# Kernel optimization log

Measured on AMD Instinct MI355X. Metric: run time of the kernel, lower is better.

## Reference

```python
import jax, jax.numpy as jnp
import numpy as np
import math

# IPA hyperparameters (AlphaFold2 / ProtSeed defaults)
H, C, PQ, PV = 12, 16, 4, 8
CS, CZ = 384, 128
INF, EPS = 1e5, 1e-8
CAT = H * (CZ + C + 4 * PV)  # 2112


def setup_inputs() -> dict:
    key = jax.random.key(0)
    ks = jax.random.split(key, 20)
    B, N = 1, 512
    s = jax.random.normal(ks[0], (B, N, CS), jnp.float32)
    z = jax.random.normal(ks[1], (B, N, N, CZ), jnp.float32)
    # valid rotation matrices via QR of random gaussians
    rot = jnp.linalg.qr(jax.random.normal(ks[2], (B, N, 3, 3), jnp.float32))[0]
    trans = jax.random.normal(ks[3], (B, N, 3), jnp.float32)
    mask = jnp.ones((B, N), jnp.float32)
    sc = 0.02
    params = {
        'w_q': jax.random.normal(ks[4], (CS, H * C), jnp.float32) * sc,
        'b_q': jnp.zeros((H * C,), jnp.float32),
        'w_kv': jax.random.normal(ks[5], (CS, 2 * H * C), jnp.float32) * sc,
        'b_kv': jnp.zeros((2 * H * C,), jnp.float32),
        'w_qp': jax.random.normal(ks[6], (CS, H * PQ * 3), jnp.float32) * sc,
        'b_qp': jnp.zeros((H * PQ * 3,), jnp.float32),
        'w_kvp': jax.random.normal(ks[7], (CS, H * (PQ + PV) * 3), jnp.float32) * sc,
        'b_kvp': jnp.zeros((H * (PQ + PV) * 3,), jnp.float32),
        'w_b': jax.random.normal(ks[8], (CZ, H), jnp.float32) * sc,
        'b_b': jnp.zeros((H,), jnp.float32),
        'head_weights': jnp.full((H,), 0.5414, jnp.float32),  # softplus^-1(1)
        'w_out': jax.random.normal(ks[9], (CAT, CS), jnp.float32) * sc,
        'b_out': jnp.zeros((CS,), jnp.float32),
    }
    return {'s': s, 'z': z, 'rot': rot, 'trans': trans, 'mask': mask, **params}


def reference(s, z, rot, trans, mask, w_q, b_q, w_kv, b_kv, w_qp, b_qp,
              w_kvp, b_kvp, w_b, b_b, head_weights, w_out, b_out):
    B, N, _ = s.shape
    w_c = math.sqrt(1.0 / (3 * C))
    w_l = math.sqrt(1.0 / 3)
    w_p = math.sqrt(1.0 / (3 * (PQ * 9.0 / 2)))

    # scalar q/k/v: [B,N,H,C]
    q = (s @ w_q + b_q).reshape(B, N, H, C)
    kv = (s @ w_kv + b_kv).reshape(B, N, H, 2 * C)
    k, v = kv[..., :C], kv[..., C:]

    # point q/k/v in global frame. torch splits the projection into 3 chunks
    # (x,y,z) along the channel dim then stacks -> [B,N,H*P,3]
    def to_pts(w, b, p):
        pts = jnp.stack(jnp.split(s @ w + b, 3, axis=-1), axis=-1)  # [B,N,H*p,3]
        pts = jnp.einsum('bnij,bnpj->bnpi', rot, pts) + trans[:, :, None, :]
        return pts.reshape(B, N, H, p, 3)

    q_pts = to_pts(w_qp, b_qp, PQ)
    kv_pts = to_pts(w_kvp, b_kvp, PQ + PV)
    k_pts, v_pts = kv_pts[..., :PQ, :], kv_pts[..., PQ:, :]

    # pair bias [B,N,N,H]
    bias = z @ w_b + b_b

    # scalar attention logits [B,H,i,j]
    a = jnp.einsum('bihc,bjhc->bhij', q, k) * w_c
    a = a + w_l * jnp.transpose(bias, (0, 3, 1, 2))

    # point-distance term: [B,i,j,H,PQ]
    d2 = jnp.sum((q_pts[:, :, None] - k_pts[:, None]) ** 2, axis=-1)
    hw = jax.nn.softplus(head_weights) * w_p
    pt_att = -0.5 * jnp.sum(d2 * hw[None, None, None, :, None], axis=-1)  # [B,i,j,H]
    a = a + jnp.transpose(pt_att, (0, 3, 1, 2))

    sq_mask = INF * (mask[:, :, None] * mask[:, None, :] - 1.0)  # [B,i,j]
    a = jax.nn.softmax(a + sq_mask[:, None], axis=-1)  # [B,H,i,j]

    # scalar output [B,N,H*C]
    o = jnp.einsum('bhij,bjhc->bihc', a, v).reshape(B, N, H * C)

    # point output, mapped back to local frames: [B,i,H,PV,3]
    o_pt = jnp.einsum('bhij,bjhpx->bihpx', a, v_pts)
    o_pt = jnp.einsum('bnji,bnhpj->bnhpi', rot, o_pt - trans[:, :, None, None, :])
    o_pt_norm = jnp.sqrt(jnp.sum(o_pt ** 2, axis=-1) + EPS).reshape(B, N, H * PV)
    o_pt = o_pt.reshape(B, N, H * PV, 3)

    # pair output [B,N,H*CZ]
    o_pair = jnp.einsum('bhij,bijc->bihc', a, z).reshape(B, N, H * CZ)

    cat = jnp.concatenate(
        [o, o_pt[..., 0], o_pt[..., 1], o_pt[..., 2], o_pt_norm, o_pair], axis=-1)
    return cat @ w_out + b_out  # [B,N,C_s]
```

## Files before the change

### kernel.cpp

```cpp
#include <hip/hip_runtime.h>
#include <math.h>

#define NN 512
#define CSd 384
#define CATd 2112
#define KF_CHUNK 264
#define KF_SPLIT 8

__global__ void k_projgemm(const float* __restrict__ s,
                           const float* __restrict__ w_q, const float* __restrict__ b_q,
                           const float* __restrict__ w_kv, const float* __restrict__ b_kv,
                           const float* __restrict__ w_qp, const float* __restrict__ b_qp,
                           const float* __restrict__ w_kvp, const float* __restrict__ b_kvp,
                           float* __restrict__ proj)
{
  __shared__ float sT[384 * 40];
  const int t  = threadIdx.x;
  const int i0 = blockIdx.x * 32;
  const int c0 = blockIdx.y * 64;

  for (int u = t; u < 32 * 384; u += 256) {
    int row = u / 384, col = u % 384;
    sT[col * 40 + row] = s[(i0 + row) * CSd + col];
  }
  __syncthreads();

  const int c    = t & 63;
  const int rgrp = t >> 6;
  const int gc   = c0 + c;

  const float* wp;
  int stride;
  float bias;
  if (gc < 192)      { wp = w_q   + gc;         stride = 192; bias = b_q[gc]; }
  else if (gc < 576) { wp = w_kv  + (gc - 192); stride = 384; bias = b_kv[gc - 192]; }
  else if (gc < 720) { wp = w_qp  + (gc - 576); stride = 144; bias = b_qp[gc - 576]; }
  else               { wp = w_kvp + (gc - 720); stride = 432; bias = b_kvp[gc - 720]; }

  float acc[8];
#pragma unroll
  for (int j = 0; j < 8; j++) acc[j] = bias;

  const int r0 = rgrp * 8;
#pragma unroll 4
  for (int kk = 0; kk < 384; kk++) {
    float wv = *wp; wp += stride;
    const float4 a0 = *reinterpret_cast<const float4*>(&sT[kk * 40 + r0]);
    const float4 a1 = *reinterpret_cast<const float4*>(&sT[kk * 40 + r0 + 4]);
    acc[0] += a0.x * wv; acc[1] += a0.y * wv; acc[2] += a0.z * wv; acc[3] += a0.w * wv;
    acc[4] += a1.x * wv; acc[5] += a1.y * wv; acc[6] += a1.z * wv; acc[7] += a1.w * wv;
  }
#pragma unroll
  for (int j = 0; j < 8; j++)
    proj[(size_t)(i0 + r0 + j) * 1152 + gc] = acc[j];
}

__global__ void k_rot(const float* __restrict__ proj,
                      const float* __restrict__ rot, const float* __restrict__ trans,
                      float* __restrict__ q, float* __restrict__ kT, float* __restrict__ vcatT,
                      float* __restrict__ qp, float* __restrict__ kpT)
{
  __shared__ float ptsL[576];
  const int i = blockIdx.x, t = threadIdx.x;
  const float* pr = proj + (size_t)i * 1152;

  for (int u = t; u < 576; u += 256) ptsL[u] = pr[576 + u];

  for (int cI = t; cI < 576; cI += 256) {
    float pv = pr[cI];
    if (cI < 192) q[i * 192 + cI] = pv;
    else {
      int local = cI - 192, h = local >> 5, cc = local & 31;
      if (cc < 16) kT[(size_t)(h * 16 + cc) * NN + i] = pv;
      else         vcatT[(size_t)(h * 16 + (cc - 16)) * NN + i] = pv;
    }
  }
  __syncthreads();

  for (int p = t; p < 192; p += 256) {
    float x, y, zz;
    if (p < 48) { x = ptsL[p]; y = ptsL[48 + p]; zz = ptsL[96 + p]; }
    else { int idx = p - 48; x = ptsL[144 + idx]; y = ptsL[288 + idx]; zz = ptsL[432 + idx]; }
    const float* Rm = rot + i * 9;
    const float* tr = trans + i * 3;
    float rx = Rm[0] * x + Rm[1] * y + Rm[2] * zz + tr[0];
    float ry = Rm[3] * x + Rm[4] * y + Rm[5] * zz + tr[1];
    float rz = Rm[6] * x + Rm[7] * y + Rm[8] * zz + tr[2];
    if (p < 48) {
      float* d = qp + ((size_t)i * 48 + p) * 3;
      d[0] = rx; d[1] = ry; d[2] = rz;
    } else {
      int idx = p - 48, h = idx / 12, pp = idx % 12;
      if (pp < 4) {
        size_t rbase = (size_t)((h * 4 + pp) * 3) * NN + i;
        kpT[rbase] = rx; kpT[rbase + NN] = ry; kpT[rbase + 2 * NN] = rz;
      } else {
        size_t rbase = (size_t)(192 + (h * 8 + pp - 4) * 3) * NN + i;
        vcatT[rbase] = rx; vcatT[rbase + NN] = ry; vcatT[rbase + 2 * NN] = rz;
      }
    }
  }
}

__global__ void k_zbias(const float* __restrict__ z, const float* __restrict__ w_b,
                        const float* __restrict__ b_b, const float* __restrict__ mask,
                        float* __restrict__ a)
{
  const int t = threadIdx.x;
  const int i = blockIdx.x >> 1;
  const int j = ((blockIdx.x & 1) << 8) + t;

  float acc[12];
#pragma unroll
  for (int h = 0; h < 12; h++) acc[h] = 0.f;

  const float4* zr = reinterpret_cast<const float4*>(z + ((size_t)i * NN + j) * 128);
#pragma unroll
  for (int b4 = 0; b4 < 4; b4++) {
    float4 zv[8];
#pragma unroll
    for (int u = 0; u < 8; u++) zv[u] = zr[b4 * 8 + u];
#pragma unroll
    for (int u = 0; u < 8; u++) {
      const int c0 = b4 * 32 + u * 4;
#pragma unroll
      for (int h = 0; h < 12; h++) {
        acc[h] += zv[u].x * w_b[(c0 + 0) * 12 + h]
                + zv[u].y * w_b[(c0 + 1) * 12 + h]
                + zv[u].z * w_b[(c0 + 2) * 12 + h]
                + zv[u].w * w_b[(c0 + 3) * 12 + h];
      }
    }
  }

  const float mterm = 100000.0f * (mask[i] * mask[j] - 1.0f);
  const float W_L = 0.57735026919f;
#pragma unroll
  for (int h = 0; h < 12; h++)
    a[((size_t)h * NN + i) * NN + j] = W_L * (acc[h] + b_b[h]) + mterm;
}

__global__ void k_qkpt(const float* __restrict__ q, const float* __restrict__ kT,
                       const float* __restrict__ qp, const float* __restrict__ kpT,
                       const float* __restrict__ hws, float* __restrict__ a)
{
  __shared__ float hwL[12];
  const int t = threadIdx.x;
  const int i = blockIdx.x >> 1;
  const int j = ((blockIdx.x & 1) << 8) + t;

  if (t < 12) hwL[t] = 0.13608276348f * log1pf(expf(hws[t]));
  __syncthreads();

  const float W_C = 0.14433756730f;
#pragma unroll 4
  for (int h = 0; h < 12; h++) {
    float dot = 0.f;
#pragma unroll
    for (int c = 0; c < 16; c++)
      dot += q[i * 192 + h * 16 + c] * kT[(size_t)(h * 16 + c) * NN + j];
    float d2 = 0.f;
#pragma unroll
    for (int pc = 0; pc < 12; pc++) {
      float dd = qp[(size_t)i * 144 + h * 12 + pc] - kpT[(size_t)(h * 12 + pc) * NN + j];
      d2 += dd * dd;
    }
    const size_t idx = ((size_t)h * NN + i) * NN + j;
    a[idx] += W_C * dot - 0.5f * hwL[h] * d2;
  }
}

__global__ void __launch_bounds__(512)
k_pvt(float* __restrict__ a, const float* __restrict__ vcatT,
      const float* __restrict__ rot, const float* __restrict__ trans,
      float* __restrict__ cat)
{
  __shared__ float PL[12 * 516];
  __shared__ float optF[288];
  const int i = blockIdx.x, t = threadIdx.x;
  const int w = t >> 6, l = t & 63;

  for (int u = t; u < 12 * 128; u += 512) {
    int h = u >> 7, c4 = u & 127;
    *reinterpret_cast<float4*>(&PL[h * 516 + c4 * 4]) =
      *reinterpret_cast<const float4*>(&a[((size_t)h * NN + i) * NN + c4 * 4]);
  }
  __syncthreads();

  for (int h = w; h < 12; h += 8) {
    float x[8];
    float m = -1e30f;
#pragma unroll
    for (int k = 0; k < 8; k++) { x[k] = PL[h * 516 + k * 64 + l]; m = fmaxf(m, x[k]); }
    for (int o = 1; o < 64; o <<= 1) m = fmaxf(m, __shfl_xor(m, o));
    float sm = 0.f;
#pragma unroll
    for (int k = 0; k < 8; k++) { x[k] = expf(x[k] - m); sm += x[k]; }
    for (int o = 1; o < 64; o <<= 1) sm += __shfl_xor(sm, o);
    float inv = 1.0f / sm;
#pragma unroll
    for (int k = 0; k < 8; k++) PL[h * 516 + k * 64 + l] = x[k] * inv;
  }
  __syncthreads();

  for (int u = t; u < 12 * 128; u += 512) {
    int h = u >> 7, c4 = u & 127;
    *reinterpret_cast<float4*>(&a[((size_t)h * NN + i) * NN + c4 * 4]) =
      *reinterpret_cast<const float4*>(&PL[h * 516 + c4 * 4]);
  }

  for (int v = w; v < 480; v += 8) {
    const int h = (v < 192) ? (v >> 4) : ((v - 192) / 24);
    const float* vr = vcatT + (size_t)v * NN;
    const float* pr = PL + h * 516;
    float acc = 0.f;
#pragma unroll
    for (int k = 0; k < 8; k++)
      acc += pr[k * 64 + l] * vr[k * 64 + l];
    for (int o = 1; o < 64; o <<= 1) acc += __shfl_xor(acc, o);
    if (l == 0) {
      if (v < 192) cat[(size_t)i * CATd + v] = acc;
      else         optF[v - 192] = acc;
    }
  }
  __syncthreads();

  if (t < 96) {
    const int h = t >> 3, p = t & 7;
    const float* Rm = rot + i * 9;
    const float* tr = trans + i * 3;
    float ox = optF[(h * 8 + p) * 3 + 0] - tr[0];
    float oy = optF[(h * 8 + p) * 3 + 1] - tr[1];
    float oz = optF[(h * 8 + p) * 3 + 2] - tr[2];
    float rx = Rm[0] * ox + Rm[3] * oy + Rm[6] * oz;
    float ry = Rm[1] * ox + Rm[4] * oy + Rm[7] * oz;
    float rz = Rm[2] * ox + Rm[5] * oy + Rm[8] * oz;
    float nrm = sqrtf(rx * rx + ry * ry + rz * rz + 1e-8f);
    size_t b = (size_t)i * CATd;
    cat[b + 192 + t] = rx; cat[b + 288 + t] = ry;
    cat[b + 384 + t] = rz; cat[b + 480 + t] = nrm;
  }
}

__global__ void k_opair(const float* __restrict__ a, const float* __restrict__ z,
                        float* __restrict__ opart)
{
  __shared__ float PL[12 * 128];
  __shared__ float red[4][64][26];
  const int jb = blockIdx.x, i = blockIdx.y;
  const int t = threadIdx.x, c2 = t & 63, jq = t >> 6;

  for (int u = t; u < 384; u += 256) {
    int h = u >> 5, c4 = u & 31;
    *reinterpret_cast<float4*>(&PL[h * 128 + c4 * 4]) =
      *reinterpret_cast<const float4*>(&a[((size_t)h * NN + i) * NN + jb * 128 + c4 * 4]);
  }
  __syncthreads();

  float acc[12][2];
#pragma unroll
  for (int h = 0; h < 12; h++) { acc[h][0] = 0.f; acc[h][1] = 0.f; }

  const int j0 = jb * 128 + jq * 32;
  const float2* zr = reinterpret_cast<const float2*>(z + ((size_t)i * NN + j0) * 128) + c2;
  for (int jj = 0; jj < 32; jj++) {
    float2 zv = zr[(size_t)jj * 64];
#pragma unroll
    for (int h = 0; h < 12; h++) {
      float pv = PL[h * 128 + jq * 32 + jj];
      acc[h][0] += pv * zv.x; acc[h][1] += pv * zv.y;
    }
  }

#pragma unroll
  for (int h = 0; h < 12; h++) {
    red[jq][c2][h * 2]     = acc[h][0];
    red[jq][c2][h * 2 + 1] = acc[h][1];
  }
  __syncthreads();

  for (int e = t; e < 1536; e += 256) {
    int h = e >> 7, c = e & 127;
    int ci = c >> 1, half = c & 1;
    float sv = red[0][ci][h * 2 + half] + red[1][ci][h * 2 + half]
             + red[2][ci][h * 2 + half] + red[3][ci][h * 2 + half];
    opart[((size_t)i * 4 + jb) * 1536 + e] = sv;
  }
}

__global__ void k_opreduce(const float* __restrict__ opart, float* __restrict__ cat)
{
  const int idx = blockIdx.x * 256 + threadIdx.x;
  const int i = idx / 1536, e = idx - i * 1536;
  const float* pb = opart + (size_t)i * 4 * 1536 + e;
  cat[(size_t)i * CATd + 576 + e] = pb[0] + pb[1536] + pb[3072] + pb[4608];
}

__global__ void k_final(const float* __restrict__ cat, const float* __restrict__ w_out,
                        float* __restrict__ part)
{
  __shared__ float sT[KF_CHUNK * 36];
  const int t  = threadIdx.x;
  const int i0 = blockIdx.x * 32;
  const int c0 = blockIdx.y * 64;
  const int k0 = blockIdx.z * KF_CHUNK;

  for (int u = t; u < 32 * KF_CHUNK; u += 256) {
    int row = u / KF_CHUNK, kk = u % KF_CHUNK;
    sT[kk * 36 + row] = cat[(size_t)(i0 + row) * CATd + k0 + kk];
  }
  __syncthreads();

  const int c    = t & 63;
  const int rgrp = t >> 6;
  const int r0   = rgrp * 8;
  const int gc   = c0 + c;

  float acc[8];
#pragma unroll
  for (int j = 0; j < 8; j++) acc[j] = 0.f;

  const float* wp = w_out + (size_t)k0 * 384 + gc;
#pragma unroll 4
  for (int kk = 0; kk < KF_CHUNK; kk++) {
    float wv = wp[(size_t)kk * 384];
    const float4 a0 = *reinterpret_cast<const float4*>(&sT[kk * 36 + r0]);
    const float4 a1 = *reinterpret_cast<const float4*>(&sT[kk * 36 + r0 + 4]);
    acc[0] += a0.x * wv; acc[1] += a0.y * wv; acc[2] += a0.z * wv; acc[3] += a0.w * wv;
    acc[4] += a1.x * wv; acc[5] += a1.y * wv; acc[6] += a1.z * wv; acc[7] += a1.w * wv;
  }

  float* pb = part + (size_t)blockIdx.z * NN * 384;
#pragma unroll
  for (int j = 0; j < 8; j++)
    pb[(size_t)(i0 + r0 + j) * 384 + gc] = acc[j];
}

__global__ void k_reduce(const float* __restrict__ part, const float* __restrict__ b_out,
                         float* __restrict__ out)
{
  const int idx = blockIdx.x * 256 + threadIdx.x;
  const int c = idx % 384;
  float acc = b_out[c];
#pragma unroll
  for (int ks = 0; ks < KF_SPLIT; ks++)
    acc += part[(size_t)ks * NN * 384 + idx];
  out[idx] = acc;
}

extern "C" void kernel_launch(void* const* d_in, const int* in_sizes, int n_in,
                              void* d_out, int out_size, void* d_ws, size_t ws_size,
                              hipStream_t stream) {
  const float* s      = (const float*)d_in[0];
  const float* z      = (const float*)d_in[1];
  const float* rot    = (const float*)d_in[2];
  const float* trans  = (const float*)d_in[3];
  const float* mask   = (const float*)d_in[4];
  const float* w_q    = (const float*)d_in[5];
  const float* b_q    = (const float*)d_in[6];
  const float* w_kv   = (const float*)d_in[7];
  const float* b_kv   = (const float*)d_in[8];
  const float* w_qp   = (const float*)d_in[9];
  const float* b_qp   = (const float*)d_in[10];
  const float* w_kvp  = (const float*)d_in[11];
  const float* b_kvp  = (const float*)d_in[12];
  const float* w_b    = (const float*)d_in[13];
  const float* b_b    = (const float*)d_in[14];
  const float* hws    = (const float*)d_in[15];
  const float* w_out  = (const float*)d_in[16];
  const float* b_out  = (const float*)d_in[17];
  float* out = (float*)d_out;

  float* ws    = (float*)d_ws;
  float* q     = ws;
  float* kT    = q     + 98304;
  float* vcatT = kT    + 98304;
  float* qp    = vcatT + 245760;
  float* kpT   = qp    + 73728;
  float* a     = kpT   + 73728;
  float* cat   = a     + 3145728;
  float* opart = cat   + 1081344;
  float* proj  = a;
  float* part  = a;

  k_projgemm<<<dim3(16, 18), 256, 0, stream>>>(s, w_q, b_q, w_kv, b_kv,
                                               w_qp, b_qp, w_kvp, b_kvp, proj);
  k_rot<<<512, 256, 0, stream>>>(proj, rot, trans, q, kT, vcatT, qp, kpT);
  k_zbias<<<1024, 256, 0, stream>>>(z, w_b, b_b, mask, a);
  k_qkpt<<<1024, 256, 0, stream>>>(q, kT, qp, kpT, hws, a);
  k_pvt<<<512, 512, 0, stream>>>(a, vcatT, rot, trans, cat);
  k_opair<<<dim3(4, 512), 256, 0, stream>>>(a, z, opart);
  k_opreduce<<<3072, 256, 0, stream>>>(opart, cat);
  k_final<<<dim3(16, 6, KF_SPLIT), 256, 0, stream>>>(cat, w_out, part);
  k_reduce<<<768, 256, 0, stream>>>(part, b_out, out);
}
```

Measured before the change: 210.9 us.

## Fuse bias, logits, softmax, value and pair outputs into one per-row kernel

Merges the z-bias, q·k/point-distance, softmax, value/point aggregation and pair-output kernels into one kernel with one block per query row i. The full attention logits for row i are built in shared memory, so the 12×512×512 attention matrix is no longer written to and re-read from global memory, and the opair partial buffer and its reduction kernel go away. z is still read twice per row (bias and pair output), but the second read may hit cache. The cost is higher register and shared-memory use per block and only 512 blocks, which may limit occupancy.

```diff
diff --git a/kernel.cpp b/kernel.cpp
--- a/kernel.cpp
+++ b/kernel.cpp
@@ -102,88 +102,70 @@
   }
 }
 
-__global__ void k_zbias(const float* __restrict__ z, const float* __restrict__ w_b,
-                        const float* __restrict__ b_b, const float* __restrict__ mask,
-                        float* __restrict__ a)
-{
-  const int t = threadIdx.x;
-  const int i = blockIdx.x >> 1;
-  const int j = ((blockIdx.x & 1) << 8) + t;
-
-  float acc[12];
-#pragma unroll
-  for (int h = 0; h < 12; h++) acc[h] = 0.f;
-
-  const float4* zr = reinterpret_cast<const float4*>(z + ((size_t)i * NN + j) * 128);
-#pragma unroll
-  for (int b4 = 0; b4 < 4; b4++) {
-    float4 zv[8];
-#pragma unroll
-    for (int u = 0; u < 8; u++) zv[u] = zr[b4 * 8 + u];
-#pragma unroll
-    for (int u = 0; u < 8; u++) {
-      const int c0 = b4 * 32 + u * 4;
-#pragma unroll
-      for (int h = 0; h < 12; h++) {
-        acc[h] += zv[u].x * w_b[(c0 + 0) * 12 + h]
-                + zv[u].y * w_b[(c0 + 1) * 12 + h]
-                + zv[u].z * w_b[(c0 + 2) * 12 + h]
-                + zv[u].w * w_b[(c0 + 3) * 12 + h];
-      }
-    }
-  }
-
-  const float mterm = 100000.0f * (mask[i] * mask[j] - 1.0f);
-  const float W_L = 0.57735026919f;
-#pragma unroll
-  for (int h = 0; h < 12; h++)
-    a[((size_t)h * NN + i) * NN + j] = W_L * (acc[h] + b_b[h]) + mterm;
-}
-
-__global__ void k_qkpt(const float* __restrict__ q, const float* __restrict__ kT,
-                       const float* __restrict__ qp, const float* __restrict__ kpT,
-                       const float* __restrict__ hws, float* __restrict__ a)
-{
-  __shared__ float hwL[12];
-  const int t = threadIdx.x;
-  const int i = blockIdx.x >> 1;
-  const int j = ((blockIdx.x & 1) << 8) + t;
-
-  if (t < 12) hwL[t] = 0.13608276348f * log1pf(expf(hws[t]));
-  __syncthreads();
-
-  const float W_C = 0.14433756730f;
-#pragma unroll 4
-  for (int h = 0; h < 12; h++) {
-    float dot = 0.f;
-#pragma unroll
-    for (int c = 0; c < 16; c++)
-      dot += q[i * 192 + h * 16 + c] * kT[(size_t)(h * 16 + c) * NN + j];
-    float d2 = 0.f;
-#pragma unroll
-    for (int pc = 0; pc < 12; pc++) {
-      float dd = qp[(size_t)i * 144 + h * 12 + pc] - kpT[(size_t)(h * 12 + pc) * NN + j];
-      d2 += dd * dd;
-    }
-    const size_t idx = ((size_t)h * NN + i) * NN + j;
-    a[idx] += W_C * dot - 0.5f * hwL[h] * d2;
-  }
-}
-
 __global__ void __launch_bounds__(512)
-k_pvt(float* __restrict__ a, const float* __restrict__ vcatT,
-      const float* __restrict__ rot, const float* __restrict__ trans,
-      float* __restrict__ cat)
-{
-  __shared__ float PL[12 * 516];
+k_fused(const float* __restrict__ z, const float* __restrict__ w_b,
+        const float* __restrict__ b_b, const float* __restrict__ mask,
+        const float* __restrict__ q, const float* __restrict__ kT,
+        const float* __restrict__ qp, const float* __restrict__ kpT,
+        const float* __restrict__ hws, const float* __restrict__ vcatT,
+        const float* __restrict__ rot, const float* __restrict__ trans,
+        float* __restrict__ cat)
+{
+  __shared__ float PL[12 * 513];
+  __shared__ float red[4][32][49];
+  __shared__ float qL[192], qpL[144], hwL[12];
   __shared__ float optF[288];
+
   const int i = blockIdx.x, t = threadIdx.x;
   const int w = t >> 6, l = t & 63;
 
-  for (int u = t; u < 12 * 128; u += 512) {
-    int h = u >> 7, c4 = u & 127;
-    *reinterpret_cast<float4*>(&PL[h * 516 + c4 * 4]) =
-      *reinterpret_cast<const float4*>(&a[((size_t)h * NN + i) * NN + c4 * 4]);
+  if (t < 192) qL[t] = q[i * 192 + t];
+  else if (t < 336) qpL[t - 192] = qp[(size_t)i * 144 + (t - 192)];
+  else if (t < 348) hwL[t - 336] = 0.13608276348f * log1pf(expf(hws[t - 336]));
+  __syncthreads();
+
+  {
+    const int j = t;
+    float acc[12];
+#pragma unroll
+    for (int h = 0; h < 12; h++) acc[h] = 0.f;
+
+    const float4* zr = reinterpret_cast<const float4*>(z + ((size_t)i * NN + j) * 128);
+#pragma unroll
+    for (int b4 = 0; b4 < 4; b4++) {
+      float4 zv[8];
+#pragma unroll
+      for (int u = 0; u < 8; u++) zv[u] = zr[b4 * 8 + u];
+#pragma unroll
+      for (int u = 0; u < 8; u++) {
+        const int c0 = b4 * 32 + u * 4;
+#pragma unroll
+        for (int h = 0; h < 12; h++) {
+          acc[h] += zv[u].x * w_b[(c0 + 0) * 12 + h]
+                  + zv[u].y * w_b[(c0 + 1) * 12 + h]
+                  + zv[u].z * w_b[(c0 + 2) * 12 + h]
+                  + zv[u].w * w_b[(c0 + 3) * 12 + h];
+        }
+      }
+    }
+
+    const float mterm = 100000.0f * (mask[i] * mask[j] - 1.0f);
+    const float W_L = 0.57735026919f;
+    const float W_C = 0.14433756730f;
+#pragma unroll 4
+    for (int h = 0; h < 12; h++) {
+      float dot = 0.f;
+#pragma unroll
+      for (int c = 0; c < 16; c++)
+        dot += qL[h * 16 + c] * kT[(size_t)(h * 16 + c) * NN + j];
+      float d2 = 0.f;
+#pragma unroll
+      for (int pc = 0; pc < 12; pc++) {
+        float dd = qpL[h * 12 + pc] - kpT[(size_t)(h * 12 + pc) * NN + j];
+        d2 += dd * dd;
+      }
+      PL[h * 513 + j] = W_L * (acc[h] + b_b[h]) + mterm + W_C * dot - 0.5f * hwL[h] * d2;
+    }
   }
   __syncthreads();
 
@@ -191,7 +173,7 @@
     float x[8];
     float m = -1e30f;
 #pragma unroll
-    for (int k = 0; k < 8; k++) { x[k] = PL[h * 516 + k * 64 + l]; m = fmaxf(m, x[k]); }
+    for (int k = 0; k < 8; k++) { x[k] = PL[h * 513 + k * 64 + l]; m = fmaxf(m, x[k]); }
     for (int o = 1; o < 64; o <<= 1) m = fmaxf(m, __shfl_xor(m, o));
     float sm = 0.f;
 #pragma unroll
@@ -199,20 +181,14 @@
     for (int o = 1; o < 64; o <<= 1) sm += __shfl_xor(sm, o);
     float inv = 1.0f / sm;
 #pragma unroll
-    for (int k = 0; k < 8; k++) PL[h * 516 + k * 64 + l] = x[k] * inv;
-  }
-  __syncthreads();
-
-  for (int u = t; u < 12 * 128; u += 512) {
-    int h = u >> 7, c4 = u & 127;
-    *reinterpret_cast<float4*>(&a[((size_t)h * NN + i) * NN + c4 * 4]) =
-      *reinterpret_cast<const float4*>(&PL[h * 516 + c4 * 4]);
-  }
+    for (int k = 0; k < 8; k++) PL[h * 513 + k * 64 + l] = x[k] * inv;
+  }
+  __syncthreads();
 
   for (int v = w; v < 480; v += 8) {
     const int h = (v < 192) ? (v >> 4) : ((v - 192) / 24);
     const float* vr = vcatT + (size_t)v * NN;
-    const float* pr = PL + h * 516;
+    const float* pr = PL + h * 513;
     float acc = 0.f;
 #pragma unroll
     for (int k = 0; k < 8; k++)
@@ -223,7 +199,58 @@
       else         optF[v - 192] = acc;
     }
   }
-  __syncthreads();
+
+  {
+    const int sub = (t >> 5) & 1;
+    const int c4  = t & 31;
+    const int jq  = t >> 6;
+    float acc[12][4];
+#pragma unroll
+    for (int h = 0; h < 12; h++)
+#pragma unroll
+      for (int c = 0; c < 4; c++) acc[h][c] = 0.f;
+
+    const float4* zb = reinterpret_cast<const float4*>(z) +
+                       ((size_t)i * NN + jq * 64 + sub) * 32 + c4;
+    const float* prow = PL + jq * 64 + sub;
+    for (int step = 0; step < 32; step++) {
+      const float4 zv = zb[(size_t)step * 64];
+      const int jo = step * 2;
+#pragma unroll
+      for (int h = 0; h < 12; h++) {
+        const float pv = prow[h * 513 + jo];
+        acc[h][0] += pv * zv.x; acc[h][1] += pv * zv.y;
+        acc[h][2] += pv * zv.z; acc[h][3] += pv * zv.w;
+      }
+    }
+#pragma unroll
+    for (int h = 0; h < 12; h++)
+#pragma unroll
+      for (int c = 0; c < 4; c++)
+        acc[h][c] += __shfl_xor(acc[h][c], 32);
+
+    if (jq >= 4 && sub == 0) {
+#pragma unroll
+      for (int h = 0; h < 12; h++)
+#pragma unroll
+        for (int c = 0; c < 4; c++) red[jq - 4][c4][h * 4 + c] = acc[h][c];
+    }
+    __syncthreads();
+    if (jq < 4 && sub == 0) {
+#pragma unroll
+      for (int h = 0; h < 12; h++)
+#pragma unroll
+        for (int c = 0; c < 4; c++) red[jq][c4][h * 4 + c] += acc[h][c];
+    }
+    __syncthreads();
+
+    for (int e = t; e < 1536; e += 512) {
+      const int h = e >> 7, c = e & 127, ci = c >> 2, cc = c & 3;
+      float sv = red[0][ci][h * 4 + cc] + red[1][ci][h * 4 + cc]
+               + red[2][ci][h * 4 + cc] + red[3][ci][h * 4 + cc];
+      cat[(size_t)i * CATd + 576 + e] = sv;
+    }
+  }
 
   if (t < 96) {
     const int h = t >> 3, p = t & 7;
@@ -240,60 +267,6 @@
     cat[b + 192 + t] = rx; cat[b + 288 + t] = ry;
     cat[b + 384 + t] = rz; cat[b + 480 + t] = nrm;
   }
-}
-
-__global__ void k_opair(const float* __restrict__ a, const float* __restrict__ z,
-                        float* __restrict__ opart)
-{
-  __shared__ float PL[12 * 128];
-  __shared__ float red[4][64][26];
-  const int jb = blockIdx.x, i = blockIdx.y;
-  const int t = threadIdx.x, c2 = t & 63, jq = t >> 6;
-
-  for (int u = t; u < 384; u += 256) {
-    int h = u >> 5, c4 = u & 31;
-    *reinterpret_cast<float4*>(&PL[h * 128 + c4 * 4]) =
-      *reinterpret_cast<const float4*>(&a[((size_t)h * NN + i) * NN + jb * 128 + c4 * 4]);
-  }
-  __syncthreads();
-
-  float acc[12][2];
-#pragma unroll
-  for (int h = 0; h < 12; h++) { acc[h][0] = 0.f; acc[h][1] = 0.f; }
-
-  const int j0 = jb * 128 + jq * 32;
-  const float2* zr = reinterpret_cast<const float2*>(z + ((size_t)i * NN + j0) * 128) + c2;
-  for (int jj = 0; jj < 32; jj++) {
-    float2 zv = zr[(size_t)jj * 64];
-#pragma unroll
-    for (int h = 0; h < 12; h++) {
-      float pv = PL[h * 128 + jq * 32 + jj];
-      acc[h][0] += pv * zv.x; acc[h][1] += pv * zv.y;
-    }
-  }
-
-#pragma unroll
-  for (int h = 0; h < 12; h++) {
-    red[jq][c2][h * 2]     = acc[h][0];
-    red[jq][c2][h * 2 + 1] = acc[h][1];
-  }
-  __syncthreads();
-
-  for (int e = t; e < 1536; e += 256) {
-    int h = e >> 7, c = e & 127;
-    int ci = c >> 1, half = c & 1;
-    float sv = red[0][ci][h * 2 + half] + red[1][ci][h * 2 + half]
-             + red[2][ci][h * 2 + half] + red[3][ci][h * 2 + half];
-    opart[((size_t)i * 4 + jb) * 1536 + e] = sv;
-  }
-}
-
-__global__ void k_opreduce(const float* __restrict__ opart, float* __restrict__ cat)
-{
-  const int idx = blockIdx.x * 256 + threadIdx.x;
-  const int i = idx / 1536, e = idx - i * 1536;
-  const float* pb = opart + (size_t)i * 4 * 1536 + e;
-  cat[(size_t)i * CATd + 576 + e] = pb[0] + pb[1536] + pb[3072] + pb[4608];
 }
 
 __global__ void k_final(const float* __restrict__ cat, const float* __restrict__ w_out,
@@ -377,20 +350,16 @@
   float* vcatT = kT    + 98304;
   float* qp    = vcatT + 245760;
   float* kpT   = qp    + 73728;
-  float* a     = kpT   + 73728;
-  float* cat   = a     + 3145728;
-  float* opart = cat   + 1081344;
-  float* proj  = a;
-  float* part  = a;
+  float* scratch = kpT + 73728;
+  float* cat   = scratch + 3145728;
+  float* proj  = scratch;
+  float* part  = scratch;
 
   k_projgemm<<<dim3(16, 18), 256, 0, stream>>>(s, w_q, b_q, w_kv, b_kv,
                                                w_qp, b_qp, w_kvp, b_kvp, proj);
   k_rot<<<512, 256, 0, stream>>>(proj, rot, trans, q, kT, vcatT, qp, kpT);
-  k_zbias<<<1024, 256, 0, stream>>>(z, w_b, b_b, mask, a);
-  k_qkpt<<<1024, 256, 0, stream>>>(q, kT, qp, kpT, hws, a);
-  k_pvt<<<512, 512, 0, stream>>>(a, vcatT, rot, trans, cat);
-  k_opair<<<dim3(4, 512), 256, 0, stream>>>(a, z, opart);
-  k_opreduce<<<3072, 256, 0, stream>>>(opart, cat);
+  k_fused<<<512, 512, 0, stream>>>(z, w_b, b_b, mask, q, kT, qp, kpT, hws,
+                                   vcatT, rot, trans, cat);
   k_final<<<dim3(16, 6, KF_SPLIT), 256, 0, stream>>>(cat, w_out, part);
   k_reduce<<<768, 256, 0, stream>>>(part, b_out, out);
 }
```

After: 215.2 us. 1.02x slower.
